# Kernel optimization log

Hardware: AMD Instinct MI355X
Metric: run time of the kernel (lower is better)

The kernel has to match this reference:

```python
import jax, jax.numpy as jnp
import numpy as np

N_CLASSES = 91  # classes 0..90; class 0 (background) is excluded from the mean


def setup_inputs() -> dict:
    key = jax.random.key(0)
    k1, k2 = jax.random.split(key)
    B, H, W = 64, 512, 512
    # label maps with integer class ids in [0, 91); `inputs` stored as float32
    # to mirror the original (compared elementwise against integer i)
    inputs = jax.random.randint(k1, (B, H, W), 0, N_CLASSES).astype(jnp.float32)
    targets = jax.random.randint(k2, (B, H, W), 0, N_CLASSES).astype(jnp.int32)
    return {"inputs": inputs, "targets": targets, "smooth": 1}


def reference(inputs, targets, smooth):
    # Single-pass histogram formulation of the original per-class loop:
    #   intersection_i = #{p : inputs[p]==i and targets[p]==i}
    #   total_i        = #{inputs==i} + #{targets==i}
    #   union_i        = total_i - intersection_i
    n = N_CLASSES
    inp = inputs.reshape(-1).astype(jnp.int32)
    tgt = targets.reshape(-1).astype(jnp.int32)
    cnt_in = jnp.bincount(inp, length=n).astype(jnp.float32)
    cnt_tg = jnp.bincount(tgt, length=n).astype(jnp.float32)
    # positions where prediction == target contribute to that class's intersection;
    # mismatches are routed to a dummy bin n and dropped
    inter = jnp.bincount(jnp.where(inp == tgt, inp, n), length=n + 1)[:n].astype(jnp.float32)
    union = cnt_in + cnt_tg - inter
    smooth_f = jnp.float32(smooth)
    iou = (inter[1:] + smooth_f) / (union[1:] + smooth_f)  # classes 1..n-1
    return jnp.sum(iou) / (n - 1)
```

## Files before the change

### kernel.cpp

```cpp
#include <hip/hip_runtime.h>

#define NCLS 91
#define NPPAD 8284
#define NHIST (3 * NCLS)
#define BS 256
#define NBLK 1024

typedef float __attribute__((ext_vector_type(4))) f32x4;
typedef int   __attribute__((ext_vector_type(4))) i32x4;

__device__ __forceinline__ void issue8(const f32x4* pf0, const f32x4* pf1,
                                       const f32x4* pf2, const f32x4* pf3,
                                       const i32x4* pt0, const i32x4* pt1,
                                       const i32x4* pt2, const i32x4* pt3,
                                       f32x4& F0, f32x4& F1, f32x4& F2, f32x4& F3,
                                       i32x4& T0, i32x4& T1, i32x4& T2, i32x4& T3) {
    asm volatile(
        "global_load_dwordx4 %0, %8, off\n\t"
        "global_load_dwordx4 %1, %9, off\n\t"
        "global_load_dwordx4 %2, %10, off\n\t"
        "global_load_dwordx4 %3, %11, off\n\t"
        "global_load_dwordx4 %4, %12, off\n\t"
        "global_load_dwordx4 %5, %13, off\n\t"
        "global_load_dwordx4 %6, %14, off\n\t"
        "global_load_dwordx4 %7, %15, off"
        : "=&v"(F0), "=&v"(F1), "=&v"(F2), "=&v"(F3),
          "=&v"(T0), "=&v"(T1), "=&v"(T2), "=&v"(T3)
        : "v"(pf0), "v"(pf1), "v"(pf2), "v"(pf3),
          "v"(pt0), "v"(pt1), "v"(pt2), "v"(pt3)
        : "memory");
}

__device__ __forceinline__ void proc16(unsigned int* __restrict__ ph,
                                       f32x4 F0, f32x4 F1, f32x4 F2, f32x4 F3,
                                       i32x4 T0, i32x4 T1, i32x4 T2, i32x4 T3) {
#define P1(F, T, c) atomicAdd(&ph[(int)F[c] * NCLS + T[c]], 1u)
#define P4(F, T) P1(F, T, 0); P1(F, T, 1); P1(F, T, 2); P1(F, T, 3)
    P4(F0, T0); P4(F1, T1); P4(F2, T2); P4(F3, T3);
#undef P4
#undef P1
}

#define WAITV(N)                                            \
    asm volatile("s_waitcnt vmcnt(" #N ")" ::: "memory");   \
    __builtin_amdgcn_sched_barrier(0)

__global__ __launch_bounds__(BS) void miou_hist(const float* __restrict__ inp,
                                                const int* __restrict__ tgt,
                                                unsigned int* __restrict__ ws) {
    __shared__ unsigned int ph[NPPAD];
    uint4* z = (uint4*)ph;
    for (int i = threadIdx.x; i < NPPAD / 4; i += BS) z[i] = make_uint4(0u, 0u, 0u, 0u);
    __syncthreads();

    const int W = blockIdx.x * 4 + (threadIdx.x >> 6);
    const int lane = threadIdx.x & 63;
    const f32x4* fb = (const f32x4*)inp;
    const i32x4* tb = (const i32x4*)tgt;
#define PF(g, u) (fb + (((W * 4 + (g)) * 4 + (u)) * 64 + lane))
#define PT(g, u) (tb + (((W * 4 + (g)) * 4 + (u)) * 64 + lane))

    f32x4 A0, A1, A2, A3, B0, B1, B2, B3;
    i32x4 A4, A5, A6, A7, B4, B5, B6, B7;

    issue8(PF(0,0), PF(0,1), PF(0,2), PF(0,3), PT(0,0), PT(0,1), PT(0,2), PT(0,3),
           A0, A1, A2, A3, A4, A5, A6, A7);
    issue8(PF(1,0), PF(1,1), PF(1,2), PF(1,3), PT(1,0), PT(1,1), PT(1,2), PT(1,3),
           B0, B1, B2, B3, B4, B5, B6, B7);
    WAITV(8);
    proc16(ph, A0, A1, A2, A3, A4, A5, A6, A7);
    issue8(PF(2,0), PF(2,1), PF(2,2), PF(2,3), PT(2,0), PT(2,1), PT(2,2), PT(2,3),
           A0, A1, A2, A3, A4, A5, A6, A7);
    WAITV(8);
    proc16(ph, B0, B1, B2, B3, B4, B5, B6, B7);
    issue8(PF(3,0), PF(3,1), PF(3,2), PF(3,3), PT(3,0), PT(3,1), PT(3,2), PT(3,3),
           B0, B1, B2, B3, B4, B5, B6, B7);
    WAITV(8);
    proc16(ph, A0, A1, A2, A3, A4, A5, A6, A7);
    WAITV(0);
    proc16(ph, B0, B1, B2, B3, B4, B5, B6, B7);
#undef PF
#undef PT
    __syncthreads();

    int t = threadIdx.x;
    if (t < NCLS) {
        const unsigned int* p = ph + t * NCLS;
        unsigned int s0 = 0, s1 = 0, s2 = 0, s3 = 0;
        int k = 0;
        for (; k + 3 < NCLS; k += 4) { s0 += p[k]; s1 += p[k+1]; s2 += p[k+2]; s3 += p[k+3]; }
        for (; k < NCLS; ++k) s0 += p[k];
        unsigned int s = s0 + s1 + s2 + s3;
        if (s) atomicAdd(&ws[t], s);
        unsigned int d = p[t];
        if (d) atomicAdd(&ws[2 * NCLS + t], d);
    } else if (t >= 128 && t < 128 + NCLS) {
        int c = t - 128;
        unsigned int s0 = 0, s1 = 0, s2 = 0, s3 = 0;
        int a = 0;
        for (; a + 3 < NCLS; a += 4) {
            s0 += ph[a * NCLS + c];
            s1 += ph[(a + 1) * NCLS + c];
            s2 += ph[(a + 2) * NCLS + c];
            s3 += ph[(a + 3) * NCLS + c];
        }
        for (; a < NCLS; ++a) s0 += ph[a * NCLS + c];
        unsigned int s = s0 + s1 + s2 + s3;
        if (s) atomicAdd(&ws[NCLS + c], s);
    }
}

__global__ __launch_bounds__(BS) void miou_hist_generic(const float* __restrict__ inp,
                                                        const int* __restrict__ tgt,
                                                        unsigned int* __restrict__ ws,
                                                        int n) {
    __shared__ unsigned int ph[NPPAD];
    uint4* z = (uint4*)ph;
    for (int i = threadIdx.x; i < NPPAD / 4; i += BS) z[i] = make_uint4(0u, 0u, 0u, 0u);
    __syncthreads();
    int stride = gridDim.x * BS;
    for (int i = blockIdx.x * BS + threadIdx.x; i < n; i += stride) {
        int a = (int)inp[i];
        int t = tgt[i];
        atomicAdd(&ph[a * NCLS + t], 1u);
    }
    __syncthreads();
    int t = threadIdx.x;
    if (t < NCLS) {
        const unsigned int* p = ph + t * NCLS;
        unsigned int s = 0;
        for (int k = 0; k < NCLS; ++k) s += p[k];
        if (s) atomicAdd(&ws[t], s);
        unsigned int d = p[t];
        if (d) atomicAdd(&ws[2 * NCLS + t], d);
    } else if (t >= 128 && t < 128 + NCLS) {
        int c = t - 128;
        unsigned int s = 0;
        for (int a = 0; a < NCLS; ++a) s += ph[a * NCLS + c];
        if (s) atomicAdd(&ws[NCLS + c], s);
    }
}

__global__ void miou_finalize(const unsigned int* __restrict__ ws,
                              const int* __restrict__ smooth_p,
                              float* __restrict__ out) {
    int lane = threadIdx.x;
    float s = (float)(*smooth_p);
    float acc = 0.f;
    for (int c = 1 + lane; c < NCLS; c += 64) {
        float ci = (float)ws[c];
        float ct = (float)ws[NCLS + c];
        float it = (float)ws[2 * NCLS + c];
        float un = ci + ct - it;
        acc += (it + s) / (un + s);
    }
    #pragma unroll
    for (int off = 32; off; off >>= 1) acc += __shfl_down(acc, off);
    if (lane == 0) out[0] = acc / (float)(NCLS - 1);
}

extern "C" void kernel_launch(void* const* d_in, const int* in_sizes, int n_in,
                              void* d_out, int out_size, void* d_ws, size_t ws_size,
                              hipStream_t stream) {
    const float* inp = (const float*)d_in[0];
    const int* tgt = (const int*)d_in[1];
    const int* smooth_p = (const int*)d_in[2];
    float* out = (float*)d_out;
    unsigned int* ws = (unsigned int*)d_ws;

    int n = in_sizes[0];
    hipMemsetAsync(ws, 0, NHIST * sizeof(unsigned int), stream);
    if (n == NBLK * 4 * 4 * 4 * 64 * 4) {
        miou_hist<<<NBLK, BS, 0, stream>>>(inp, tgt, ws);
    } else {
        miou_hist_generic<<<1024, BS, 0, stream>>>(inp, tgt, ws, n);
    }
    miou_finalize<<<1, 64, 0, stream>>>(ws, smooth_p, out);
}
```

Baseline: 157.4 us.

## Replace shared-memory atomic histogram with per-thread packed private histograms

The hot path drops LDS atomicAdd on a shared 91x91 joint histogram. Each thread now keeps private counters in LDS, laid out class-major. A 16-bit slot per class packs the prediction count (low byte) and the intersection count (high byte), and an 8-bit slot holds the target count; they are updated with plain read-modify-write. Each block now processes twice as many elements over half as many blocks, with a longer double-buffered load pipeline. Global accumulation is spread over 8 shards that the finalize kernel sums. The aim is to remove atomic serialization and contention in LDS. In exchange, each element now costs two LDS loads and two stores, and the roughly 70 KB of LDS per block limits occupancy. The 8-bit counters also depend on each thread handling at most 255 elements.

After: 154.6 us. No clear change (-1.8%).

```diff
diff --git a/kernel.cpp b/kernel.cpp
--- a/kernel.cpp
+++ b/kernel.cpp
@@ -1,10 +1,11 @@
 #include <hip/hip_runtime.h>
 
 #define NCLS 91
-#define NPPAD 8284
-#define NHIST (3 * NCLS)
+#define TPB 256
+#define NSHARD 8
 #define BS 256
-#define NBLK 1024
+#define NBLK 512
+#define GENS 8
 
 typedef float __attribute__((ext_vector_type(4))) f32x4;
 typedef int   __attribute__((ext_vector_type(4))) i32x4;
@@ -31,14 +32,22 @@
         : "memory");
 }
 
-__device__ __forceinline__ void proc16(unsigned int* __restrict__ ph,
-                                       f32x4 F0, f32x4 F1, f32x4 F2, f32x4 F3,
-                                       i32x4 T0, i32x4 T1, i32x4 T2, i32x4 T3) {
-#define P1(F, T, c) atomicAdd(&ph[(int)F[c] * NCLS + T[c]], 1u)
-#define P4(F, T) P1(F, T, 0); P1(F, T, 1); P1(F, T, 2); P1(F, T, 3)
-    P4(F0, T0); P4(F1, T1); P4(F2, T2); P4(F3, T3);
-#undef P4
-#undef P1
+__device__ __forceinline__ void rmw16(unsigned short* __restrict__ h16,
+                                      unsigned char* __restrict__ tg8, int tid,
+                                      f32x4 F0, f32x4 F1, f32x4 F2, f32x4 F3,
+                                      i32x4 T0, i32x4 T1, i32x4 T2, i32x4 T3) {
+#define E1(F, Tv, c)                                                          \
+    {                                                                         \
+        int a = (int)F[c];                                                    \
+        int tv = Tv[c];                                                       \
+        h16[a * TPB + tid] =                                                  \
+            (unsigned short)(h16[a * TPB + tid] + 1u + ((a == tv) << 8));     \
+        tg8[tv * TPB + tid] = (unsigned char)(tg8[tv * TPB + tid] + 1u);      \
+    }
+#define E4(F, Tv) E1(F, Tv, 0) E1(F, Tv, 1) E1(F, Tv, 2) E1(F, Tv, 3)
+    E4(F0, T0) E4(F1, T1) E4(F2, T2) E4(F3, T3)
+#undef E4
+#undef E1
 }
 
 #define WAITV(N)                                            \
@@ -48,65 +57,74 @@
 __global__ __launch_bounds__(BS) void miou_hist(const float* __restrict__ inp,
                                                 const int* __restrict__ tgt,
                                                 unsigned int* __restrict__ ws) {
-    __shared__ unsigned int ph[NPPAD];
-    uint4* z = (uint4*)ph;
-    for (int i = threadIdx.x; i < NPPAD / 4; i += BS) z[i] = make_uint4(0u, 0u, 0u, 0u);
+    __shared__ unsigned short h16[NCLS * TPB];
+    __shared__ unsigned char  tg8[NCLS * TPB];
+    uint4* z1 = (uint4*)h16;
+    uint4* z2 = (uint4*)tg8;
+    for (int i = threadIdx.x; i < NCLS * TPB * 2 / 16; i += BS) z1[i] = make_uint4(0,0,0,0);
+    for (int i = threadIdx.x; i < NCLS * TPB / 16; i += BS) z2[i] = make_uint4(0,0,0,0);
     __syncthreads();
 
-    const int W = blockIdx.x * 4 + (threadIdx.x >> 6);
-    const int lane = threadIdx.x & 63;
+    const int tid = threadIdx.x;
+    const int W = blockIdx.x * 4 + (tid >> 6);
+    const int lane = tid & 63;
     const f32x4* fb = (const f32x4*)inp;
     const i32x4* tb = (const i32x4*)tgt;
-#define PF(g, u) (fb + (((W * 4 + (g)) * 4 + (u)) * 64 + lane))
-#define PT(g, u) (tb + (((W * 4 + (g)) * 4 + (u)) * 64 + lane))
+#define PF(g, u) (fb + (((W * GENS + (g)) * 4 + (u)) * 64 + lane))
+#define PT(g, u) (tb + (((W * GENS + (g)) * 4 + (u)) * 64 + lane))
+#define ISSUE(BK, g) issue8(PF(g,0), PF(g,1), PF(g,2), PF(g,3),               \
+                            PT(g,0), PT(g,1), PT(g,2), PT(g,3),               \
+                            BK##0, BK##1, BK##2, BK##3, BK##4, BK##5, BK##6, BK##7)
+#define PROC(BK) rmw16(h16, tg8, tid, BK##0, BK##1, BK##2, BK##3, BK##4, BK##5, BK##6, BK##7)
 
     f32x4 A0, A1, A2, A3, B0, B1, B2, B3;
     i32x4 A4, A5, A6, A7, B4, B5, B6, B7;
 
-    issue8(PF(0,0), PF(0,1), PF(0,2), PF(0,3), PT(0,0), PT(0,1), PT(0,2), PT(0,3),
-           A0, A1, A2, A3, A4, A5, A6, A7);
-    issue8(PF(1,0), PF(1,1), PF(1,2), PF(1,3), PT(1,0), PT(1,1), PT(1,2), PT(1,3),
-           B0, B1, B2, B3, B4, B5, B6, B7);
-    WAITV(8);
-    proc16(ph, A0, A1, A2, A3, A4, A5, A6, A7);
-    issue8(PF(2,0), PF(2,1), PF(2,2), PF(2,3), PT(2,0), PT(2,1), PT(2,2), PT(2,3),
-           A0, A1, A2, A3, A4, A5, A6, A7);
-    WAITV(8);
-    proc16(ph, B0, B1, B2, B3, B4, B5, B6, B7);
-    issue8(PF(3,0), PF(3,1), PF(3,2), PF(3,3), PT(3,0), PT(3,1), PT(3,2), PT(3,3),
-           B0, B1, B2, B3, B4, B5, B6, B7);
-    WAITV(8);
-    proc16(ph, A0, A1, A2, A3, A4, A5, A6, A7);
-    WAITV(0);
-    proc16(ph, B0, B1, B2, B3, B4, B5, B6, B7);
+    ISSUE(A, 0); ISSUE(B, 1);
+    WAITV(8); PROC(A); ISSUE(A, 2);
+    WAITV(8); PROC(B); ISSUE(B, 3);
+    WAITV(8); PROC(A); ISSUE(A, 4);
+    WAITV(8); PROC(B); ISSUE(B, 5);
+    WAITV(8); PROC(A); ISSUE(A, 6);
+    WAITV(8); PROC(B); ISSUE(B, 7);
+    WAITV(8); PROC(A);
+    WAITV(0); PROC(B);
 #undef PF
 #undef PT
+#undef ISSUE
+#undef PROC
     __syncthreads();
 
+    const int shard = (blockIdx.x & (NSHARD - 1)) * 3 * NCLS;
     int t = threadIdx.x;
     if (t < NCLS) {
-        const unsigned int* p = ph + t * NCLS;
-        unsigned int s0 = 0, s1 = 0, s2 = 0, s3 = 0;
-        int k = 0;
-        for (; k + 3 < NCLS; k += 4) { s0 += p[k]; s1 += p[k+1]; s2 += p[k+2]; s3 += p[k+3]; }
-        for (; k < NCLS; ++k) s0 += p[k];
-        unsigned int s = s0 + s1 + s2 + s3;
-        if (s) atomicAdd(&ws[t], s);
-        unsigned int d = p[t];
-        if (d) atomicAdd(&ws[2 * NCLS + t], d);
+        const uint4* row = (const uint4*)&h16[t * TPB];
+        unsigned int cin = 0, cit = 0;
+        #pragma unroll 4
+        for (int k = 0; k < 32; ++k) {
+            uint4 v = row[k];
+            unsigned int d;
+            d = v.x; cin += (d & 0xFFu) + ((d >> 16) & 0xFFu); cit += ((d >> 8) & 0xFFu) + (d >> 24);
+            d = v.y; cin += (d & 0xFFu) + ((d >> 16) & 0xFFu); cit += ((d >> 8) & 0xFFu) + (d >> 24);
+            d = v.z; cin += (d & 0xFFu) + ((d >> 16) & 0xFFu); cit += ((d >> 8) & 0xFFu) + (d >> 24);
+            d = v.w; cin += (d & 0xFFu) + ((d >> 16) & 0xFFu); cit += ((d >> 8) & 0xFFu) + (d >> 24);
+        }
+        if (cin) atomicAdd(&ws[shard + t], cin);
+        if (cit) atomicAdd(&ws[shard + 2 * NCLS + t], cit);
     } else if (t >= 128 && t < 128 + NCLS) {
         int c = t - 128;
-        unsigned int s0 = 0, s1 = 0, s2 = 0, s3 = 0;
-        int a = 0;
-        for (; a + 3 < NCLS; a += 4) {
-            s0 += ph[a * NCLS + c];
-            s1 += ph[(a + 1) * NCLS + c];
-            s2 += ph[(a + 2) * NCLS + c];
-            s3 += ph[(a + 3) * NCLS + c];
+        const uint4* row = (const uint4*)&tg8[c * TPB];
+        unsigned int s = 0;
+        #pragma unroll 4
+        for (int k = 0; k < 16; ++k) {
+            uint4 v = row[k];
+            unsigned int d;
+            d = v.x; s += (d & 0xFFu) + ((d >> 8) & 0xFFu) + ((d >> 16) & 0xFFu) + (d >> 24);
+            d = v.y; s += (d & 0xFFu) + ((d >> 8) & 0xFFu) + ((d >> 16) & 0xFFu) + (d >> 24);
+            d = v.z; s += (d & 0xFFu) + ((d >> 8) & 0xFFu) + ((d >> 16) & 0xFFu) + (d >> 24);
+            d = v.w; s += (d & 0xFFu) + ((d >> 8) & 0xFFu) + ((d >> 16) & 0xFFu) + (d >> 24);
         }
-        for (; a < NCLS; ++a) s0 += ph[a * NCLS + c];
-        unsigned int s = s0 + s1 + s2 + s3;
-        if (s) atomicAdd(&ws[NCLS + c], s);
+        if (s) atomicAdd(&ws[shard + NCLS + c], s);
     }
 }
 
@@ -114,9 +132,9 @@
                                                         const int* __restrict__ tgt,
                                                         unsigned int* __restrict__ ws,
                                                         int n) {
-    __shared__ unsigned int ph[NPPAD];
+    __shared__ unsigned int ph[NCLS * NCLS + 3];
     uint4* z = (uint4*)ph;
-    for (int i = threadIdx.x; i < NPPAD / 4; i += BS) z[i] = make_uint4(0u, 0u, 0u, 0u);
+    for (int i = threadIdx.x; i < (NCLS * NCLS + 3) / 4; i += BS) z[i] = make_uint4(0,0,0,0);
     __syncthreads();
     int stride = gridDim.x * BS;
     for (int i = blockIdx.x * BS + threadIdx.x; i < n; i += stride) {
@@ -127,11 +145,10 @@
     __syncthreads();
     int t = threadIdx.x;
     if (t < NCLS) {
-        const unsigned int* p = ph + t * NCLS;
         unsigned int s = 0;
-        for (int k = 0; k < NCLS; ++k) s += p[k];
+        for (int k = 0; k < NCLS; ++k) s += ph[t * NCLS + k];
         if (s) atomicAdd(&ws[t], s);
-        unsigned int d = p[t];
+        unsigned int d = ph[t * NCLS + t];
         if (d) atomicAdd(&ws[2 * NCLS + t], d);
     } else if (t >= 128 && t < 128 + NCLS) {
         int c = t - 128;
@@ -148,11 +165,14 @@
     float s = (float)(*smooth_p);
     float acc = 0.f;
     for (int c = 1 + lane; c < NCLS; c += 64) {
-        float ci = (float)ws[c];
-        float ct = (float)ws[NCLS + c];
-        float it = (float)ws[2 * NCLS + c];
-        float un = ci + ct - it;
-        acc += (it + s) / (un + s);
+        float ci = 0.f, ct = 0.f, it = 0.f;
+        #pragma unroll
+        for (int sh = 0; sh < NSHARD; ++sh) {
+            ci += (float)ws[sh * 3 * NCLS + c];
+            ct += (float)ws[sh * 3 * NCLS + NCLS + c];
+            it += (float)ws[sh * 3 * NCLS + 2 * NCLS + c];
+        }
+        acc += (it + s) / (ci + ct - it + s);
     }
     #pragma unroll
     for (int off = 32; off; off >>= 1) acc += __shfl_down(acc, off);
@@ -169,8 +189,8 @@
     unsigned int* ws = (unsigned int*)d_ws;
 
     int n = in_sizes[0];
-    hipMemsetAsync(ws, 0, NHIST * sizeof(unsigned int), stream);
-    if (n == NBLK * 4 * 4 * 4 * 64 * 4) {
+    hipMemsetAsync(ws, 0, NSHARD * 3 * NCLS * sizeof(unsigned int), stream);
+    if (n == NBLK * 4 * GENS * 4 * 64 * 4) {
         miou_hist<<<NBLK, BS, 0, stream>>>(inp, tgt, ws);
     } else {
         miou_hist_generic<<<1024, BS, 0, stream>>>(inp, tgt, ws, n);
```
